# Kernel optimization log

Hardware: AMD Instinct MI355X
Metric: run time of the kernel (lower is better)

The kernel has to match this reference:

```python
import jax, jax.numpy as jnp
import numpy as np

B, T, V, H = 128, 1024, 256, 512  # batch, max seq len, vocab_count, latent_dim
PAD_VALUE = 0.0  # pad_index = 0 used as padding_value in pad_packed_sequence


def setup_inputs() -> dict:
    key = jax.random.key(0)
    k_x, k_len, k_wi, k_wh, k_bi, k_bh = jax.random.split(key, 6)
    x = jax.random.randint(k_x, (B, T), 0, V, dtype=jnp.int32)
    x_len = jax.random.randint(k_len, (B,), 1, T + 1, dtype=jnp.int32)
    x_len = x_len.at[0].set(T)  # ensure padded output length == T (static shape)
    s = 0.05
    W_ih = jax.random.normal(k_wi, (4 * H, V), dtype=jnp.float32) * s
    W_hh = jax.random.normal(k_wh, (4 * H, H), dtype=jnp.float32) * s
    b_ih = jax.random.normal(k_bi, (4 * H,), dtype=jnp.float32) * s
    b_hh = jax.random.normal(k_bh, (4 * H,), dtype=jnp.float32) * s
    return {"x": x, "x_len": x_len, "W_ih": W_ih, "W_hh": W_hh,
            "b_ih": b_ih, "b_hh": b_hh}


def _lstm_packed(x, x_len, W_ih, W_hh, b_ih, b_hh):
    # one-hot input projection (mathematically == embedding gather W_ih.T[x])
    oh = jax.nn.one_hot(x, W_ih.shape[1], dtype=W_ih.dtype)          # [B,T,V]
    proj = jnp.einsum('btv,gv->btg', oh, W_ih) + b_ih + b_hh         # [B,T,4H]
    proj_t = jnp.transpose(proj, (1, 0, 2))                          # [T,B,4H]
    # mask[t,b] = True while t < x_len[b] (packed-sequence semantics)
    mask_t = jnp.arange(proj.shape[1])[:, None] < x_len[None, :]     # [T,B]

    h0 = jnp.zeros((x.shape[0], W_hh.shape[1]), dtype=W_ih.dtype)
    c0 = jnp.zeros_like(h0)

    def step(carry, inp):
        h, c = carry
        p, m = inp                                                   # [B,4H],[B]
        gates = p + h @ W_hh.T
        i, f, g, o = jnp.split(gates, 4, axis=-1)                    # torch order i,f,g,o
        i = jax.nn.sigmoid(i)
        f = jax.nn.sigmoid(f)
        g = jnp.tanh(g)
        o = jax.nn.sigmoid(o)
        c_new = f * c + i * g
        h_new = o * jnp.tanh(c_new)
        m1 = m[:, None]
        h = jnp.where(m1, h_new, h)   # freeze state past each sequence's length
        c = jnp.where(m1, c_new, c)
        out = jnp.where(m1, h_new, PAD_VALUE)  # padding_value = pad_index
        return (h, c), out

    (h_T, c_T), ys = jax.lax.scan(step, (h0, c0), (proj_t, mask_t))
    output = jnp.transpose(ys, (1, 0, 2))                            # [B,T,H]
    return output, h_T, c_T


def reference(x, x_len, W_ih, W_hh, b_ih, b_hh):
    output, h_T, c_T = _lstm_packed(x, x_len, W_ih, W_hh, b_ih, b_hh)
    # hidden/cell shaped [num_layers*num_dirs=1, B, H] like torch LSTM
    return output, h_T[None], c_T[None]
```

## Files before the change

kernel.cpp:

```cpp
#include <hip/hip_runtime.h>
#include <hip/hip_bf16.h>


#define TT 1024
#define BB 128
#define HH 512
#define VV 256
#define NGP 8
#define GM 16
#define NWG 8
#define NE 64
#define FSTRIDE 32

typedef __attribute__((ext_vector_type(8))) short short8;
typedef __attribute__((ext_vector_type(4))) float f32x4;
typedef unsigned long long u64;
typedef unsigned short u16;

__device__ __forceinline__ u16 f2bf(float f) {
  __hip_bfloat16 h = __float2bfloat16(f);
  return *reinterpret_cast<u16*>(&h);
}
__device__ __forceinline__ float sigm(float x) { return 1.0f / (1.0f + __expf(-x)); }
__device__ __forceinline__ float tanh_(float x) { return 1.0f - 2.0f / (1.0f + __expf(2.0f * x)); }

__global__ void lstm_init(const int* __restrict__ x, int* __restrict__ x_t,
                          unsigned int* __restrict__ hbuf0, int* __restrict__ flags) {
  int idx = blockIdx.x * 256 + threadIdx.x;
  int t = idx >> 7, b = idx & 127;
  x_t[idx] = x[b * TT + t];
  if (idx < (BB * HH / 2)) hbuf0[idx] = 0u;
  if (idx < NGP * NWG * FSTRIDE) flags[idx] = 0;
}

__launch_bounds__(256, 1)
__global__ void lstm_persist(const int* __restrict__ x_t, const int* __restrict__ x_len,
                             const float* __restrict__ W_ih, const float* __restrict__ W_hh,
                             const float* __restrict__ b_ih, const float* __restrict__ b_hh,
                             float* __restrict__ out,
                             u16* __restrict__ hbuf,
                             int* __restrict__ flags) {
  const int tid = threadIdx.x;
  const int wave = tid >> 6, lane = tid & 63;
  const int nn = lane & 15, quad = lane >> 4;
  const int g = blockIdx.x >> 3, ig = blockIdx.x & 7;

  __shared__ u16 hA[GM * 520];
  __shared__ float gates_s[GM * 260];
  __shared__ u16 hstage[GM * NE];

  short8 bw[4][16];
#pragma unroll
  for (int s = 0; s < 4; s++) {
    const float* src = W_hh + (size_t)(wave * HH + ig * NE + s * 16 + nn) * HH + quad * 8;
#pragma unroll
    for (int kt = 0; kt < 16; kt++) {
      const float* p = src + kt * 32;
      short8 v;
#pragma unroll
      for (int j = 0; j < 8; j++) v[j] = (short)f2bf(p[j]);
      bw[s][kt] = v;
    }
  }

  const int bc = tid >> 4, e4 = (tid & 15) * 4;
  const int bglob = g * GM + bc;
  const int xl = x_len[bglob];
  float bias[4][4];
#pragma unroll
  for (int q = 0; q < 4; q++)
#pragma unroll
    for (int j = 0; j < 4; j++) {
      int grow = q * HH + ig * NE + e4 + j;
      bias[q][j] = b_ih[grow] + b_hh[grow];
    }
  float cst[4] = {0.f, 0.f, 0.f, 0.f}, hst[4] = {0.f, 0.f, 0.f, 0.f};

  const int srow = tid >> 4, scol = (tid & 15) * 32;
  const u64 stage_off = (u64)(((g * GM + srow) * HH + scol) * 2);

  int* flmine = flags + (g * NWG + ig) * FSTRIDE;
  const int* flpoll = flags + (g * NWG + (lane & 7)) * FSTRIDE;

  __syncthreads();

  for (int t = 0; t < TT; ++t) {
    const int slot = t & 1;

    const int xv = x_t[t * BB + bglob];
    float w[4][4];
#pragma unroll
    for (int q = 0; q < 4; q++)
#pragma unroll
      for (int j = 0; j < 4; j++)
        w[q][j] = W_ih[(size_t)(q * HH + ig * NE + e4 + j) * VV + xv];

    if (wave == 0) {
      while (true) {
        int v = __hip_atomic_load(flpoll, __ATOMIC_RELAXED, __HIP_MEMORY_SCOPE_AGENT);
        if (__all(v >= t)) break;
        __builtin_amdgcn_s_sleep(1);
      }
    }
    __syncthreads();

    {
      u64 gsrc = (u64)(hbuf + (size_t)slot * (BB * HH)) + stage_off;
      short8 t0, t1, t2, t3;
      asm volatile(
          "global_load_dwordx4 %0, %4, off sc1\n\t"
          "global_load_dwordx4 %1, %4, off offset:16 sc1\n\t"
          "global_load_dwordx4 %2, %4, off offset:32 sc1\n\t"
          "global_load_dwordx4 %3, %4, off offset:48 sc1\n\t"
          "s_waitcnt vmcnt(0)"
          : "=&v"(t0), "=&v"(t1), "=&v"(t2), "=&v"(t3)
          : "v"(gsrc)
          : "memory");
      short8* dst = (short8*)(hA + srow * 520 + scol);
      dst[0] = t0; dst[1] = t1; dst[2] = t2; dst[3] = t3;
    }
    __syncthreads();

    {
      f32x4 acc[4] = {{0,0,0,0},{0,0,0,0},{0,0,0,0},{0,0,0,0}};
      const u16* ap = hA + nn * 520 + quad * 8;
#pragma unroll
      for (int kt = 0; kt < 16; kt++) {
        short8 a = *(const short8*)(ap + kt * 32);
#pragma unroll
        for (int s = 0; s < 4; s++)
          acc[s] = __builtin_amdgcn_mfma_f32_16x16x32_bf16(a, bw[s][kt], acc[s], 0, 0, 0);
      }
#pragma unroll
      for (int s = 0; s < 4; s++)
#pragma unroll
        for (int r = 0; r < 4; r++)
          gates_s[(quad * 4 + r) * 260 + wave * NE + s * 16 + nn] = acc[s][r];
    }
    __syncthreads();

    {
      f32x4 G0 = *(const f32x4*)&gates_s[bc * 260 + 0 * NE + e4];
      f32x4 G1 = *(const f32x4*)&gates_s[bc * 260 + 1 * NE + e4];
      f32x4 G2 = *(const f32x4*)&gates_s[bc * 260 + 2 * NE + e4];
      f32x4 G3 = *(const f32x4*)&gates_s[bc * 260 + 3 * NE + e4];
      const bool act = (t < xl);
      f32x4 outv;
#pragma unroll
      for (int j = 0; j < 4; j++) {
        float gi = G0[j] + w[0][j] + bias[0][j];
        float gf = G1[j] + w[1][j] + bias[1][j];
        float gg = G2[j] + w[2][j] + bias[2][j];
        float go = G3[j] + w[3][j] + bias[3][j];
        float iv = sigm(gi), fv = sigm(gf), gv = tanh_(gg), ov = sigm(go);
        float cn = fv * cst[j] + iv * gv;
        float hn = ov * tanh_(cn);
        if (act) { cst[j] = cn; hst[j] = hn; }
        outv[j] = act ? hn : 0.0f;
        hstage[bc * NE + e4 + j] = f2bf(hst[j]);
      }
      *(f32x4*)&out[((size_t)bglob * TT + t) * HH + ig * NE + e4] = outv;
    }
    __syncthreads();

    if (wave == 0) {
      const u64* hs = (const u64*)hstage;
      u64 v0 = hs[lane * 4], v1 = hs[lane * 4 + 1], v2 = hs[lane * 4 + 2], v3 = hs[lane * 4 + 3];
      int row = lane >> 2, cin = (lane * 4) & 15;
      u64* dst = (u64*)(hbuf + (size_t)(slot ^ 1) * (BB * HH)
                        + (size_t)(g * GM + row) * HH + ig * NE + cin * 4);
      __hip_atomic_store(dst + 0, v0, __ATOMIC_RELAXED, __HIP_MEMORY_SCOPE_AGENT);
      __hip_atomic_store(dst + 1, v1, __ATOMIC_RELAXED, __HIP_MEMORY_SCOPE_AGENT);
      __hip_atomic_store(dst + 2, v2, __ATOMIC_RELAXED, __HIP_MEMORY_SCOPE_AGENT);
      __hip_atomic_store(dst + 3, v3, __ATOMIC_RELAXED, __HIP_MEMORY_SCOPE_AGENT);
      asm volatile("s_waitcnt vmcnt(0)" ::: "memory");
      if (lane == 0)
        __hip_atomic_store(flmine, t + 1, __ATOMIC_RELAXED, __HIP_MEMORY_SCOPE_AGENT);
    }
  }

  {
    f32x4 hv, cv;
#pragma unroll
    for (int j = 0; j < 4; j++) { hv[j] = hst[j]; cv[j] = cst[j]; }
    *(f32x4*)&out[(size_t)BB * TT * HH + (size_t)bglob * HH + ig * NE + e4] = hv;
    *(f32x4*)&out[(size_t)BB * TT * HH + (size_t)BB * HH + (size_t)bglob * HH + ig * NE + e4] = cv;
  }
}

extern "C" void kernel_launch(void* const* d_in, const int* in_sizes, int n_in,
                              void* d_out, int out_size, void* d_ws, size_t ws_size,
                              hipStream_t stream) {
  const int*   x     = (const int*)d_in[0];
  const int*   x_len = (const int*)d_in[1];
  const float* W_ih  = (const float*)d_in[2];
  const float* W_hh  = (const float*)d_in[3];
  const float* b_ih  = (const float*)d_in[4];
  const float* b_hh  = (const float*)d_in[5];
  float* out = (float*)d_out;

  char* ws = (char*)d_ws;
  int* x_t = (int*)ws;
  u16* hbuf = (u16*)(ws + 524288);
  int* flags = (int*)(ws + 524288 + 262144);

  lstm_init<<<512, 256, 0, stream>>>(x, x_t, (unsigned int*)hbuf, flags);
  lstm_persist<<<64, 256, 0, stream>>>(x_t, x_len, W_ih, W_hh, b_ih, b_hh, out, hbuf, flags);
}
```

Baseline: 5.816 ms.

## Stop each batch group at its max length and streamline cross-block h exchange

Each workgroup group computes the maximum sequence length among its 16 batch rows, runs the recurrence only up to that step, and afterwards writes zero padding for the remaining steps. The h handoff now has every thread store its own bf16 h packet directly to global memory, replacing the LDS staging buffer and the single-wave store. Flag polling is spread across lanes in every wave instead of one wave followed by a barrier. The h loads are reorganised into strided 16-byte chunks, and output stores become nontemporal. The aim is to skip padded timesteps and cut barrier and serialization cost per step, at the price of every thread waiting on its own store before the flag is published.

```diff
diff --git a/kernel.cpp b/kernel.cpp
--- a/kernel.cpp
+++ b/kernel.cpp
@@ -47,7 +47,7 @@
 
   __shared__ u16 hA[GM * 520];
   __shared__ float gates_s[GM * 260];
-  __shared__ u16 hstage[GM * NE];
+  __shared__ int gmax_s;
 
   short8 bw[4][16];
 #pragma unroll
@@ -76,15 +76,19 @@
     }
   float cst[4] = {0.f, 0.f, 0.f, 0.f}, hst[4] = {0.f, 0.f, 0.f, 0.f};
 
-  const int srow = tid >> 4, scol = (tid & 15) * 32;
-  const u64 stage_off = (u64)(((g * GM + srow) * HH + scol) * 2);
+  if (tid == 0) gmax_s = 1;
+  __syncthreads();
+  if ((tid & 15) == 0) atomicMax(&gmax_s, xl);
+
+  const int srow = tid >> 4, sc16 = tid & 15;
+  const u64 stage_off = (u64)((size_t)(g * GM + srow) * HH * 2 + (size_t)sc16 * 16);
 
   int* flmine = flags + (g * NWG + ig) * FSTRIDE;
-  const int* flpoll = flags + (g * NWG + (lane & 7)) * FSTRIDE;
 
   __syncthreads();
-
-  for (int t = 0; t < TT; ++t) {
+  const int gmax = gmax_s;
+
+  for (int t = 0; t < gmax; ++t) {
     const int slot = t & 1;
 
     const int xv = x_t[t * BB + bglob];
@@ -95,29 +99,26 @@
       for (int j = 0; j < 4; j++)
         w[q][j] = W_ih[(size_t)(q * HH + ig * NE + e4 + j) * VV + xv];
 
-    if (wave == 0) {
-      while (true) {
-        int v = __hip_atomic_load(flpoll, __ATOMIC_RELAXED, __HIP_MEMORY_SCOPE_AGENT);
-        if (__all(v >= t)) break;
+    if (lane < 8 && lane != ig) {
+      const int* fp = flags + (g * NWG + lane) * FSTRIDE;
+      while (__hip_atomic_load(fp, __ATOMIC_RELAXED, __HIP_MEMORY_SCOPE_AGENT) < t)
         __builtin_amdgcn_s_sleep(1);
-      }
-    }
-    __syncthreads();
+    }
 
     {
       u64 gsrc = (u64)(hbuf + (size_t)slot * (BB * HH)) + stage_off;
       short8 t0, t1, t2, t3;
       asm volatile(
           "global_load_dwordx4 %0, %4, off sc1\n\t"
-          "global_load_dwordx4 %1, %4, off offset:16 sc1\n\t"
-          "global_load_dwordx4 %2, %4, off offset:32 sc1\n\t"
-          "global_load_dwordx4 %3, %4, off offset:48 sc1\n\t"
+          "global_load_dwordx4 %1, %4, off offset:256 sc1\n\t"
+          "global_load_dwordx4 %2, %4, off offset:512 sc1\n\t"
+          "global_load_dwordx4 %3, %4, off offset:768 sc1\n\t"
           "s_waitcnt vmcnt(0)"
           : "=&v"(t0), "=&v"(t1), "=&v"(t2), "=&v"(t3)
           : "v"(gsrc)
           : "memory");
-      short8* dst = (short8*)(hA + srow * 520 + scol);
-      dst[0] = t0; dst[1] = t1; dst[2] = t2; dst[3] = t3;
+      short8* dst = (short8*)(hA + srow * 520 + sc16 * 8);
+      dst[0] = t0; dst[16] = t1; dst[32] = t2; dst[48] = t3;
     }
     __syncthreads();
 
@@ -157,26 +158,27 @@
         float hn = ov * tanh_(cn);
         if (act) { cst[j] = cn; hst[j] = hn; }
         outv[j] = act ? hn : 0.0f;
-        hstage[bc * NE + e4 + j] = f2bf(hst[j]);
       }
-      *(f32x4*)&out[((size_t)bglob * TT + t) * HH + ig * NE + e4] = outv;
+      u64 hword = (u64)f2bf(hst[0]) | ((u64)f2bf(hst[1]) << 16)
+                | ((u64)f2bf(hst[2]) << 32) | ((u64)f2bf(hst[3]) << 48);
+      u64* hdst = (u64*)(hbuf + (size_t)(slot ^ 1) * (BB * HH)
+                         + (size_t)bglob * HH + ig * NE + e4);
+      __hip_atomic_store(hdst, hword, __ATOMIC_RELAXED, __HIP_MEMORY_SCOPE_AGENT);
+      asm volatile("s_waitcnt vmcnt(0)" ::: "memory");
+      __builtin_nontemporal_store(outv,
+          (f32x4*)&out[((size_t)bglob * TT + t) * HH + ig * NE + e4]);
     }
     __syncthreads();
 
-    if (wave == 0) {
-      const u64* hs = (const u64*)hstage;
-      u64 v0 = hs[lane * 4], v1 = hs[lane * 4 + 1], v2 = hs[lane * 4 + 2], v3 = hs[lane * 4 + 3];
-      int row = lane >> 2, cin = (lane * 4) & 15;
-      u64* dst = (u64*)(hbuf + (size_t)(slot ^ 1) * (BB * HH)
-                        + (size_t)(g * GM + row) * HH + ig * NE + cin * 4);
-      __hip_atomic_store(dst + 0, v0, __ATOMIC_RELAXED, __HIP_MEMORY_SCOPE_AGENT);
-      __hip_atomic_store(dst + 1, v1, __ATOMIC_RELAXED, __HIP_MEMORY_SCOPE_AGENT);
-      __hip_atomic_store(dst + 2, v2, __ATOMIC_RELAXED, __HIP_MEMORY_SCOPE_AGENT);
-      __hip_atomic_store(dst + 3, v3, __ATOMIC_RELAXED, __HIP_MEMORY_SCOPE_AGENT);
-      asm volatile("s_waitcnt vmcnt(0)" ::: "memory");
-      if (lane == 0)
-        __hip_atomic_store(flmine, t + 1, __ATOMIC_RELAXED, __HIP_MEMORY_SCOPE_AGENT);
-    }
+    if (tid == 0)
+      __hip_atomic_store(flmine, t + 1, __ATOMIC_RELAXED, __HIP_MEMORY_SCOPE_AGENT);
+  }
+
+  {
+    f32x4 z = {0.f, 0.f, 0.f, 0.f};
+    for (int t = gmax; t < TT; ++t)
+      __builtin_nontemporal_store(z,
+          (f32x4*)&out[((size_t)bglob * TT + t) * HH + ig * NE + e4]);
   }
 
   {
```

After: 5.436 ms. 1.07x faster.
